# Optimization experiments

Hardware: AMD Instinct MI355X
Metric: run time of the kernel (lower is better)

Reference implementation:

```python
import jax, jax.numpy as jnp
import numpy as np

BATCH = 8
IN_FEATURES = 4096
OUT_FEATURES = 16384


def setup_inputs() -> dict:
    key = jax.random.key(0)
    k1, k2, k3 = jax.random.split(key, 3)
    # activations, fp16 (w4a16 path)
    x = jax.random.normal(k1, (BATCH, IN_FEATURES), dtype=jnp.float16)
    # packed int4 weights: each element holds two signed 4-bit values
    # (low nibble = even column 2k, high nibble = odd column 2k+1)
    weight = jax.random.randint(k2, (OUT_FEATURES, IN_FEATURES // 2), 0, 256, dtype=jnp.int32)
    # per-output-channel symmetric scales (small positive values)
    weight_scales = (jax.random.uniform(k3, (OUT_FEATURES,), dtype=jnp.float16) * jnp.float16(0.01)
                     + jnp.float16(0.001))
    return {"x": x, "weight": weight, "weight_scales": weight_scales}


def _dequant_i4(weight, scales):
    """Unpack two signed int4 per byte and apply per-row scales.
    weight: [out, in//2] int32 (byte values 0..255); scales: [out] fp16.
    Returns [out, in] in scales.dtype.
    """
    low = weight & 0xF
    high = (weight >> 4) & 0xF
    # sign-extend 4-bit two's complement (the torch module stores signed int4;
    # mask 0x88 XOR in the kernel is the equivalent sign-bit flip)
    low = jnp.where(low >= 8, low - 16, low)
    high = jnp.where(high >= 8, high - 16, high)
    w = jnp.stack([low, high], axis=-1).reshape(weight.shape[0], -1)  # [out, in]
    return w.astype(scales.dtype) * scales[:, None]


def reference(x, weight, weight_scales):
    W = _dequant_i4(weight, weight_scales)           # [out, in] fp16
    return jnp.matmul(x, W.T)                         # [batch, out] fp16
```

## Files before the change

### kernel.cpp

```cpp
#include <hip/hip_runtime.h>
#include <hip/hip_bf16.h>
#include <stdint.h>

#define BATCH 8
#define K_DIM 4096
#define N_DIM 16384
#define KH (K_DIM / 2)
#define BLOCK 512
#define ROWS_PER_WAVE 4
#define ROWS_PER_BLOCK 32
#define ITERS 8

typedef __attribute__((ext_vector_type(2))) float f32x2;
typedef __attribute__((ext_vector_type(4))) int   i32x4;
typedef __attribute__((ext_vector_type(4))) uint  u32x4;

__device__ __forceinline__ float bf16lo(uint32_t u) { return __uint_as_float(u << 16); }
__device__ __forceinline__ float bf16hi(uint32_t u) { return __uint_as_float(u & 0xFFFF0000u); }

__device__ __forceinline__ uint32_t f32_to_bf16_bits(float f) {
    uint32_t u = __float_as_uint(f);
    return (u + 0x7FFFu + ((u >> 16) & 1u)) >> 16;
}

__global__ __launch_bounds__(BLOCK, 2)
void w4a16_gemv(const float* __restrict__ x,
                const int*   __restrict__ w,
                const float* __restrict__ scales,
                float*       __restrict__ out)
{
    __shared__ u32x4 xchunks[K_DIM];
    const int tid = threadIdx.x;

    #pragma unroll
    for (int t = 0; t < K_DIM / BLOCK; ++t) {
        const int c = t * BLOCK + tid;
        float v[BATCH];
        #pragma unroll
        for (int b = 0; b < BATCH; ++b) v[b] = x[b * K_DIM + c];
        u32x4 pk;
        pk.x = f32_to_bf16_bits(v[0]) | (f32_to_bf16_bits(v[1]) << 16);
        pk.y = f32_to_bf16_bits(v[2]) | (f32_to_bf16_bits(v[3]) << 16);
        pk.z = f32_to_bf16_bits(v[4]) | (f32_to_bf16_bits(v[5]) << 16);
        pk.w = f32_to_bf16_bits(v[6]) | (f32_to_bf16_bits(v[7]) << 16);
        xchunks[c ^ ((c >> 3) & 7)] = pk;
    }
    __syncthreads();

    const int wave = tid >> 6;
    const int lane = tid & 63;
    const int row0 = blockIdx.x * ROWS_PER_BLOCK + wave * ROWS_PER_WAVE;
    const int xork = lane & 7;
    const int lbase = lane << 3;

    const i32x4* __restrict__ wv0 = (const i32x4*)(w + (size_t)(row0 + 0) * KH);
    const i32x4* __restrict__ wv1 = (const i32x4*)(w + (size_t)(row0 + 1) * KH);
    const i32x4* __restrict__ wv2 = (const i32x4*)(w + (size_t)(row0 + 2) * KH);
    const i32x4* __restrict__ wv3 = (const i32x4*)(w + (size_t)(row0 + 3) * KH);

    f32x2 acc2[ROWS_PER_WAVE][BATCH / 2];
    #pragma unroll
    for (int j = 0; j < ROWS_PER_WAVE; ++j)
        #pragma unroll
        for (int p = 0; p < BATCH / 2; ++p) acc2[j][p] = (f32x2){0.0f, 0.0f};

    i32x4 q[3][ROWS_PER_WAVE];

#define LOADQ(s, tt)                                                          \
    {                                                                         \
        const int u_ = ((tt) << 6) + lane;                                    \
        q[s][0] = wv0[u_];                                                    \
        q[s][1] = wv1[u_];                                                    \
        q[s][2] = wv2[u_];                                                    \
        q[s][3] = wv3[u_];                                                    \
    }

    LOADQ(0, 0)
    LOADQ(1, 1)

    #pragma unroll
    for (int t = 0; t < ITERS; ++t) {
        if (t + 2 < ITERS) LOADQ((t + 2) % 3, t + 2)

        const int s = t % 3;
        #pragma unroll
        for (int m = 0; m < 4; ++m) {
            const u32x4 xa = xchunks[lbase + ((2 * m)     ^ xork) + t * 512];
            const u32x4 xb = xchunks[lbase + ((2 * m + 1) ^ xork) + t * 512];
            f32x2 xlo2[4], xhi2[4];
            xlo2[0] = (f32x2){bf16lo(xa.x), bf16hi(xa.x)};
            xlo2[1] = (f32x2){bf16lo(xa.y), bf16hi(xa.y)};
            xlo2[2] = (f32x2){bf16lo(xa.z), bf16hi(xa.z)};
            xlo2[3] = (f32x2){bf16lo(xa.w), bf16hi(xa.w)};
            xhi2[0] = (f32x2){bf16lo(xb.x), bf16hi(xb.x)};
            xhi2[1] = (f32x2){bf16lo(xb.y), bf16hi(xb.y)};
            xhi2[2] = (f32x2){bf16lo(xb.z), bf16hi(xb.z)};
            xhi2[3] = (f32x2){bf16lo(xb.w), bf16hi(xb.w)};

            int qm[ROWS_PER_WAVE];
            qm[0] = q[s][0][m];
            qm[1] = q[s][1][m];
            qm[2] = q[s][2][m];
            qm[3] = q[s][3][m];

            #pragma unroll
            for (int j = 0; j < ROWS_PER_WAVE; ++j) {
                const uint32_t bv = ((uint32_t)qm[j]) & 0xFFu;
                const float flo = (float)((int)(bv << 28) >> 28);
                const float fhi = (float)((int)(bv << 24) >> 28);
                const f32x2 flo2 = (f32x2){flo, flo};
                const f32x2 fhi2 = (f32x2){fhi, fhi};
                #pragma unroll
                for (int p = 0; p < BATCH / 2; ++p) {
                    acc2[j][p] = __builtin_elementwise_fma(flo2, xlo2[p], acc2[j][p]);
                    acc2[j][p] = __builtin_elementwise_fma(fhi2, xhi2[p], acc2[j][p]);
                }
            }
        }
    }
#undef LOADQ

    float vals[32];
    #pragma unroll
    for (int j = 0; j < ROWS_PER_WAVE; ++j)
        #pragma unroll
        for (int p = 0; p < BATCH / 2; ++p) {
            vals[j * 8 + 2 * p]     = acc2[j][p].x;
            vals[j * 8 + 2 * p + 1] = acc2[j][p].y;
        }

    #pragma unroll
    for (int k = 0; k < 5; ++k) {
        const int sel = (lane >> k) & 1;
        const int n = 32 >> k;
        #pragma unroll
        for (int i = 0; i < n / 2; ++i) {
            const float a = vals[2 * i];
            const float c = vals[2 * i + 1];
            const float mine  = sel ? c : a;
            const float other = sel ? a : c;
            vals[i] = mine + __shfl_xor(other, 1 << k, 64);
        }
    }
    const float total = vals[0] + __shfl_xor(vals[0], 32, 64);

    if (lane < 32) {
        const int r = row0 + (lane >> 3);
        out[(size_t)(lane & 7) * N_DIM + r] = total * scales[r];
    }
}

extern "C" void kernel_launch(void* const* d_in, const int* in_sizes, int n_in,
                              void* d_out, int out_size, void* d_ws, size_t ws_size,
                              hipStream_t stream) {
    const float* x      = (const float*)d_in[0];
    const int*   w      = (const int*)d_in[1];
    const float* scales = (const float*)d_in[2];
    float*       out    = (float*)d_out;

    dim3 grid(N_DIM / ROWS_PER_BLOCK);
    dim3 block(BLOCK);
    hipLaunchKernelGGL(w4a16_gemv, grid, block, 0, stream, x, w, scales, out);
}
```

Measured before the change: 208.7 us.

## Halve rows per wave and issue all weight loads before staging x

Each wave now handles 2 output rows instead of 4, so the grid doubles to 1024 blocks. All 8 iterations of weight loads for both rows are issued at kernel entry into registers, before the x conversion into shared memory and the barrier. This hides weight-fetch latency behind the x staging work instead of relying on a 3-stage rolling prefetch. The cost is that every block redoes the x conversion and LDS fill for half as many rows, and the larger register footprint for the 16 preloaded vectors may reduce occupancy. The reduction tree is adjusted to 16 values plus two cross-lane shuffles.

```diff
diff --git a/kernel.cpp b/kernel.cpp
--- a/kernel.cpp
+++ b/kernel.cpp
@@ -7,8 +7,8 @@
 #define N_DIM 16384
 #define KH (K_DIM / 2)
 #define BLOCK 512
-#define ROWS_PER_WAVE 4
-#define ROWS_PER_BLOCK 32
+#define ROWS_PER_WAVE 2
+#define ROWS_PER_BLOCK 16
 #define ITERS 8
 
 typedef __attribute__((ext_vector_type(2))) float f32x2;
@@ -32,6 +32,20 @@
     __shared__ u32x4 xchunks[K_DIM];
     const int tid = threadIdx.x;
 
+    const int wave = tid >> 6;
+    const int lane = tid & 63;
+    const int row0 = blockIdx.x * ROWS_PER_BLOCK + wave * ROWS_PER_WAVE;
+
+    const i32x4* __restrict__ wv0 = (const i32x4*)(w + (size_t)(row0 + 0) * KH) + lane;
+    const i32x4* __restrict__ wv1 = (const i32x4*)(w + (size_t)(row0 + 1) * KH) + lane;
+
+    i32x4 q0[ITERS], q1[ITERS];
+    #pragma unroll
+    for (int t = 0; t < ITERS; ++t) {
+        q0[t] = wv0[t * 64];
+        q1[t] = wv1[t * 64];
+    }
+
     #pragma unroll
     for (int t = 0; t < K_DIM / BLOCK; ++t) {
         const int c = t * BLOCK + tid;
@@ -47,16 +61,8 @@
     }
     __syncthreads();
 
-    const int wave = tid >> 6;
-    const int lane = tid & 63;
-    const int row0 = blockIdx.x * ROWS_PER_BLOCK + wave * ROWS_PER_WAVE;
-    const int xork = lane & 7;
+    const int xork  = lane & 7;
     const int lbase = lane << 3;
-
-    const i32x4* __restrict__ wv0 = (const i32x4*)(w + (size_t)(row0 + 0) * KH);
-    const i32x4* __restrict__ wv1 = (const i32x4*)(w + (size_t)(row0 + 1) * KH);
-    const i32x4* __restrict__ wv2 = (const i32x4*)(w + (size_t)(row0 + 2) * KH);
-    const i32x4* __restrict__ wv3 = (const i32x4*)(w + (size_t)(row0 + 3) * KH);
 
     f32x2 acc2[ROWS_PER_WAVE][BATCH / 2];
     #pragma unroll
@@ -64,25 +70,8 @@
         #pragma unroll
         for (int p = 0; p < BATCH / 2; ++p) acc2[j][p] = (f32x2){0.0f, 0.0f};
 
-    i32x4 q[3][ROWS_PER_WAVE];
-
-#define LOADQ(s, tt)                                                          \
-    {                                                                         \
-        const int u_ = ((tt) << 6) + lane;                                    \
-        q[s][0] = wv0[u_];                                                    \
-        q[s][1] = wv1[u_];                                                    \
-        q[s][2] = wv2[u_];                                                    \
-        q[s][3] = wv3[u_];                                                    \
-    }
-
-    LOADQ(0, 0)
-    LOADQ(1, 1)
-
     #pragma unroll
     for (int t = 0; t < ITERS; ++t) {
-        if (t + 2 < ITERS) LOADQ((t + 2) % 3, t + 2)
-
-        const int s = t % 3;
         #pragma unroll
         for (int m = 0; m < 4; ++m) {
             const u32x4 xa = xchunks[lbase + ((2 * m)     ^ xork) + t * 512];
@@ -97,11 +86,7 @@
             xhi2[2] = (f32x2){bf16lo(xb.z), bf16hi(xb.z)};
             xhi2[3] = (f32x2){bf16lo(xb.w), bf16hi(xb.w)};
 
-            int qm[ROWS_PER_WAVE];
-            qm[0] = q[s][0][m];
-            qm[1] = q[s][1][m];
-            qm[2] = q[s][2][m];
-            qm[3] = q[s][3][m];
+            const int qm[ROWS_PER_WAVE] = { q0[t][m], q1[t][m] };
 
             #pragma unroll
             for (int j = 0; j < ROWS_PER_WAVE; ++j) {
@@ -118,9 +103,8 @@
             }
         }
     }
-#undef LOADQ
 
-    float vals[32];
+    float vals[16];
     #pragma unroll
     for (int j = 0; j < ROWS_PER_WAVE; ++j)
         #pragma unroll
@@ -130,9 +114,9 @@
         }
 
     #pragma unroll
-    for (int k = 0; k < 5; ++k) {
+    for (int k = 0; k < 4; ++k) {
         const int sel = (lane >> k) & 1;
-        const int n = 32 >> k;
+        const int n = 16 >> k;
         #pragma unroll
         for (int i = 0; i < n / 2; ++i) {
             const float a = vals[2 * i];
@@ -142,9 +126,10 @@
             vals[i] = mine + __shfl_xor(other, 1 << k, 64);
         }
     }
-    const float total = vals[0] + __shfl_xor(vals[0], 32, 64);
+    float t1    = vals[0] + __shfl_xor(vals[0], 16, 64);
+    float total = t1      + __shfl_xor(t1,      32, 64);
 
-    if (lane < 32) {
+    if (lane < 16) {
         const int r = row0 + (lane >> 3);
         out[(size_t)(lane & 7) * N_DIM + r] = total * scales[r];
     }
```

Result: no change. 212.1 us (+1.6%).
